# Kernel optimization log

Hardware: AMD Instinct MI355X
Metric: run time of the kernel (lower is better)

## Reference

```python
import jax, jax.numpy as jnp
import numpy as np

N_HEADS = 16
D_KV = 64
NUM_BUCKETS = 64      # bidirectional T5 buckets
MAX_DISTANCE = 50     # hist_step


def _rel_bucket(rel_pos):
    # T5 bidirectional relative-position bucketing.
    nb = NUM_BUCKETS // 2
    ret = (rel_pos > 0).astype(jnp.int32) * nb
    n = jnp.abs(rel_pos)
    max_exact = nb // 2
    is_small = n < max_exact
    large = max_exact + (
        jnp.log(jnp.maximum(n, 1).astype(jnp.float32) / max_exact)
        / np.log(MAX_DISTANCE / max_exact)
        * (nb - max_exact)
    ).astype(jnp.int32)
    large = jnp.minimum(large, nb - 1)
    return ret + jnp.where(is_small, n, large)


def _position_bias(rel_table, qlen, klen):
    ctx = jnp.arange(qlen)[:, None]
    mem = jnp.arange(klen)[None, :]
    bucket = _rel_bucket(mem - ctx)            # (q, k)
    vals = rel_table[bucket]                   # (q, k, h)
    return jnp.transpose(vals, (2, 0, 1))[None]  # (1, h, q, k)


def setup_inputs() -> dict:
    key = jax.random.key(0)
    ks = jax.random.split(key, 11)
    bs, qlen, d_model = 2, 2048, 1024
    inner = N_HEADS * D_KV
    s = 0.02
    return {
        "x": jax.random.normal(ks[0], (bs, qlen, d_model), jnp.float32),
        "Wq": jax.random.normal(ks[1], (d_model, inner), jnp.float32) * s,
        "bq": jnp.zeros((inner,), jnp.float32),
        "Wk": jax.random.normal(ks[2], (d_model, inner), jnp.float32) * s,
        "bk": jnp.zeros((inner,), jnp.float32),
        "Wv": jax.random.normal(ks[3], (d_model, inner), jnp.float32) * s,
        "bv": jnp.zeros((inner,), jnp.float32),
        "Wo": jax.random.normal(ks[4], (inner, d_model), jnp.float32) * s,
        "bo": jnp.zeros((d_model,), jnp.float32),
        "rel_table": jax.random.normal(ks[5], (NUM_BUCKETS, N_HEADS), jnp.float32) * s,
        "mask": jax.random.randint(ks[6], (bs, qlen), 0, 2) > 0,
    }


def reference(x, Wq, bq, Wk, bk, Wv, bv, Wo, bo, rel_table, mask):
    bs, qlen, d_model = x.shape

    def shape(h):  # (b, s, inner) -> (b, n, s, d)
        return h.reshape(bs, qlen, N_HEADS, D_KV).transpose(0, 2, 1, 3)

    q = shape(x @ Wq + bq)
    k = shape(x @ Wk + bk)
    v = shape(x @ Wv + bv)

    # No 1/sqrt(d) scaling in T5.
    scores = jnp.einsum('bnqd,bnkd->bnqk', q, k)

    mask_f = jnp.where(mask, -jnp.inf, 0.0).astype(scores.dtype)[:, None, None, :]  # (b,1,1,k)
    pos_bias = _position_bias(rel_table, qlen, qlen)  # (1,h,q,k)
    add = pos_bias + mask_f                           # bias + mask, broadcast over q

    weights = jax.nn.softmax(scores + add, axis=-1)   # dropout p=0 -> identity
    context = jnp.einsum('bnqk,bnkd->bnqd', weights, v)
    context = context.transpose(0, 2, 1, 3).reshape(bs, qlen, N_HEADS * D_KV)
    out = context @ Wo + bo
    return out, weights, pos_bias
```

## Files before the change

kernel.cpp:

```cpp
#include <hip/hip_runtime.h>
#include <math.h>

typedef _Float16 f16;
typedef f16 f16x8 __attribute__((ext_vector_type(8)));
typedef f16 f16x4 __attribute__((ext_vector_type(4)));
typedef float f32x4 __attribute__((ext_vector_type(4)));

#define W_OFF   (2*2048*1024)
#define PB_OFF  (W_OFF + 2LL*16*2048*2048)

#define NEG_BIG (-1.0e30f)

__device__ __forceinline__ int rel_bucket(int rel) {
    int ret = rel > 0 ? 32 : 0;
    int n = rel < 0 ? -rel : rel;
    if (n < 16) return ret + n;
    float fn = (float)n;
    float t = logf(fn * (1.0f / 16.0f));
    t = t / 1.1394343f;
    int large = 16 + (int)(t * 16.0f);
    if (large > 31) large = 31;
    return ret + large;
}


__global__ __launch_bounds__(256)
void conv_f16_kernel(const float* __restrict__ in, f16* __restrict__ out) {
    size_t i = ((size_t)blockIdx.x * 256 + threadIdx.x) * 4;
    float4 v = *(const float4*)&in[i];
    f16x4 h = { (f16)v.x, (f16)v.y, (f16)v.z, (f16)v.w };
    *(f16x4*)&out[i] = h;
}

__global__ __launch_bounds__(256)
void transpose_w_kernel(const float* __restrict__ W, f16* __restrict__ Wt) {
    __shared__ float tile[64 * 68];
    const int tid = threadIdx.x;
    const int bi = blockIdx.x, bj = blockIdx.y;
    #pragma unroll
    for (int it = 0; it < 4; ++it) {
        int slot = tid + it * 256;
        int row = slot >> 4, col4 = (slot & 15) * 4;
        float4 v = *(const float4*)&W[(size_t)(bi * 64 + row) * 1024 + bj * 64 + col4];
        *(float4*)&tile[row * 68 + col4] = v;
    }
    __syncthreads();
    #pragma unroll
    for (int it = 0; it < 4; ++it) {
        int slot = tid + it * 256;
        int nrow = slot >> 4, kcol4 = (slot & 15) * 4;
        f16x4 h;
        #pragma unroll
        for (int j = 0; j < 4; ++j)
            h[j] = (f16)tile[(kcol4 + j) * 68 + nrow];
        *(f16x4*)&Wt[(size_t)(bj * 64 + nrow) * 1024 + bi * 64 + kcol4] = h;
    }
}

__global__ __launch_bounds__(256)
void bias_tbl_kernel(const float* __restrict__ rel_table, float* __restrict__ tbl) {
    int idx = blockIdx.x * 256 + threadIdx.x;
    int h = idx >> 12, dd = idx & 4095;
    tbl[idx] = rel_table[rel_bucket(dd - 2047) * 16 + h];
}

__global__ __launch_bounds__(256)
void transpose_v_kernel(const f16* __restrict__ vh, f16* __restrict__ vt) {
    __shared__ f16 tile[64 * 72];
    const int tid = threadIdx.x;
    const int st = blockIdx.x, bh = blockIdx.y;
    #pragma unroll
    for (int it = 0; it < 2; ++it) {
        int slot = tid + it * 256;
        int row = slot >> 3, col8 = (slot & 7) * 8;
        f16x8 v = *(const f16x8*)&vh[((size_t)bh * 2048 + st * 64 + row) * 64 + col8];
        *(f16x8*)&tile[row * 72 + col8] = v;
    }
    __syncthreads();
    #pragma unroll
    for (int it = 0; it < 2; ++it) {
        int slot = tid + it * 256;
        int drow = slot >> 3, scol8 = (slot & 7) * 8;
        f16x8 r;
        #pragma unroll
        for (int j = 0; j < 8; ++j)
            r[j] = tile[(scol8 + j) * 72 + drow];
        *(f16x8*)&vt[((size_t)bh * 64 + drow) * 2048 + st * 64 + scol8] = r;
    }
}

__global__ __launch_bounds__(256)
void gemm_f16(const f16* __restrict__ A, const f16* __restrict__ Bt,
              const float* __restrict__ bias, void* __restrict__ Cout, int mode)
{
    __shared__ f16 aLDS[128 * 32];
    __shared__ f16 bLDS[128 * 32];
    const int tid = threadIdx.x;
    const int lane = tid & 63, wv = tid >> 6;
    const int quad = lane >> 4, l15 = lane & 15;
    const int wm = (wv & 1) * 64, wn = (wv >> 1) * 64;
    const int bm = blockIdx.y * 128, bn = blockIdx.x * 128;

    f32x4 acc[4][4];
    #pragma unroll
    for (int i = 0; i < 4; ++i)
        #pragma unroll
        for (int j = 0; j < 4; ++j)
            acc[i][j] = (f32x4){0.f, 0.f, 0.f, 0.f};

    for (int k0 = 0; k0 < 1024; k0 += 32) {
        __syncthreads();
        #pragma unroll
        for (int s = 0; s < 2; ++s) {
            int slot = tid + s * 256;
            int mt = slot >> 6, ln = slot & 63;
            int row = mt * 16 + (ln & 15), kk = (ln >> 4) * 8;
            float4 va = *(const float4*)&A[(size_t)(bm + row) * 1024 + k0 + kk];
            *(float4*)&aLDS[slot * 8] = va;
            float4 vb = *(const float4*)&Bt[(size_t)(bn + row) * 1024 + k0 + kk];
            *(float4*)&bLDS[slot * 8] = vb;
        }
        __syncthreads();
        f16x8 af[4], bf[4];
        #pragma unroll
        for (int i = 0; i < 4; ++i) {
            af[i] = *(const f16x8*)&aLDS[(((wm >> 4) + i) * 64 + lane) * 8];
            bf[i] = *(const f16x8*)&bLDS[(((wn >> 4) + i) * 64 + lane) * 8];
        }
        #pragma unroll
        for (int i = 0; i < 4; ++i)
            #pragma unroll
            for (int j = 0; j < 4; ++j)
                acc[i][j] = __builtin_amdgcn_mfma_f32_16x16x32_f16(af[i], bf[j], acc[i][j], 0, 0, 0);
    }

    #pragma unroll
    for (int j = 0; j < 4; ++j) {
        int n = bn + wn + j * 16 + l15;
        float bz = bias[n];
        #pragma unroll
        for (int i = 0; i < 4; ++i) {
            #pragma unroll
            for (int r = 0; r < 4; ++r) {
                int m = bm + wm + i * 16 + quad * 4 + r;
                float val = acc[i][j][r] + bz;
                if (mode == 0) {
                    ((float*)Cout)[(size_t)m * 1024 + n] = val;
                } else {
                    int b = m >> 11, srow = m & 2047, h = n >> 6, d = n & 63;
                    ((f16*)Cout)[(((size_t)(b * 16 + h) * 2048 + srow) << 6) + d] = (f16)val;
                }
            }
        }
    }
}

__global__ __launch_bounds__(256)
void attn_f16(const f16* __restrict__ qh, const f16* __restrict__ kh,
              const f16* __restrict__ vth, const float* __restrict__ tbl,
              const int* __restrict__ mask, float* __restrict__ wout,
              f16* __restrict__ ctxh)
{
    __shared__ float biasL[4096];
    __shared__ float maskL[2048];
    __shared__ f16 kL[8 * 64 * 8];
    __shared__ f16 vL[8 * 64 * 8];
    __shared__ f16 wnat[4 * 16 * 88];

    const int tid = threadIdx.x, lane = tid & 63, wv = tid >> 6;
    const int quad = lane >> 4, l15 = lane & 15;
    const int bh = blockIdx.y, b = bh >> 4, h = bh & 15;
    const int qt0 = blockIdx.x * 64;

    for (int i = tid; i < 1024; i += 256)
        *(float4*)&biasL[i * 4] = *(const float4*)&tbl[h * 4096 + i * 4];
    for (int i = tid; i < 512; i += 256) {
        int4 mv = *(const int4*)&mask[b * 2048 + i * 4];
        float4 f;
        f.x = mv.x ? NEG_BIG : 0.f;  f.y = mv.y ? NEG_BIG : 0.f;
        f.z = mv.z ? NEG_BIG : 0.f;  f.w = mv.w ? NEG_BIG : 0.f;
        *(float4*)&maskL[i * 4] = f;
    }

    const int q0 = qt0 + wv * 16;
    f16x8 aq[2];
    #pragma unroll
    for (int ds = 0; ds < 2; ++ds)
        aq[ds] = *(const f16x8*)&qh[((size_t)bh * 2048 + q0 + l15) * 64 + ds * 32 + quad * 8];
    __syncthreads();

    const int qrow_base = q0 + quad * 4;
    float lI[4] = {0.f, 0.f, 0.f, 0.f};

    for (int c = 0; c < 32; ++c) {
        __syncthreads();
        #pragma unroll
        for (int s = 0; s < 2; ++s) {
            int slot = tid + s * 256;
            int f = slot >> 6, ln = slot & 63;
            int dstep = f >> 2, nt = f & 3;
            int key = nt * 16 + (ln & 15);
            float4 v = *(const float4*)&kh[((size_t)bh * 2048 + c * 64 + key) * 64 + dstep * 32 + (ln >> 4) * 8];
            *(float4*)&kL[slot * 8] = v;
        }
        __syncthreads();
        #pragma unroll
        for (int nt = 0; nt < 4; ++nt) {
            f32x4 s4 = (f32x4){0.f, 0.f, 0.f, 0.f};
            #pragma unroll
            for (int ds = 0; ds < 2; ++ds) {
                f16x8 bf = *(const f16x8*)&kL[((ds * 4 + nt) * 64 + lane) * 8];
                s4 = __builtin_amdgcn_mfma_f32_16x16x32_f16(aq[ds], bf, s4, 0, 0, 0);
            }
            int k = c * 64 + nt * 16 + l15;
            float mk = maskL[k];
            #pragma unroll
            for (int r = 0; r < 4; ++r) {
                int q = qrow_base + r;
                float sc = s4[r] + biasL[k - q + 2047] + mk;
                lI[r] += __expf(sc - 20.f);
            }
        }
    }
    #pragma unroll
    for (int r = 0; r < 4; ++r) {
        float l = lI[r];
        l += __shfl_xor(l, 1, 64);
        l += __shfl_xor(l, 2, 64);
        l += __shfl_xor(l, 4, 64);
        l += __shfl_xor(l, 8, 64);
        lI[r] = 1.0f / l;
    }

    float* wbase = wout + (size_t)bh * 2048 * 2048;
    f32x4 oacc[4];
    #pragma unroll
    for (int nt = 0; nt < 4; ++nt) oacc[nt] = (f32x4){0.f, 0.f, 0.f, 0.f};

    for (int c = 0; c < 32; ++c) {
        __syncthreads();
        #pragma unroll
        for (int s = 0; s < 2; ++s) {
            int slot = tid + s * 256;
            int f = slot >> 6, ln = slot & 63;
            {
                int dstep = f >> 2, nt = f & 3;
                int key = nt * 16 + (ln & 15);
                float4 v = *(const float4*)&kh[((size_t)bh * 2048 + c * 64 + key) * 64 + dstep * 32 + (ln >> 4) * 8];
                *(float4*)&kL[slot * 8] = v;
            }
            {
                int ks = f >> 2, nt = f & 3;
                int d = nt * 16 + (ln & 15);
                float4 v = *(const float4*)&vth[((size_t)bh * 64 + d) * 2048 + c * 64 + ks * 32 + (ln >> 4) * 8];
                *(float4*)&vL[slot * 8] = v;
            }
        }
        __syncthreads();

        #pragma unroll
        for (int nt = 0; nt < 4; ++nt) {
            f32x4 s4 = (f32x4){0.f, 0.f, 0.f, 0.f};
            #pragma unroll
            for (int ds = 0; ds < 2; ++ds) {
                f16x8 bf = *(const f16x8*)&kL[((ds * 4 + nt) * 64 + lane) * 8];
                s4 = __builtin_amdgcn_mfma_f32_16x16x32_f16(aq[ds], bf, s4, 0, 0, 0);
            }
            int k = c * 64 + nt * 16 + l15;
            float mk = maskL[k];
            int key64 = nt * 16 + l15;
            #pragma unroll
            for (int r = 0; r < 4; ++r) {
                int q = qrow_base + r;
                float sc = s4[r] + biasL[k - q + 2047] + mk;
                float w = __expf(sc - 20.f) * lI[r];
                wbase[(size_t)q * 2048 + k] = w;
                wnat[wv * 1408 + (quad * 4 + r) * 88 + key64] = (f16)w;
            }
        }
        #pragma unroll
        for (int ks = 0; ks < 2; ++ks) {
            f16x8 wf = *(const f16x8*)&wnat[wv * 1408 + l15 * 88 + ks * 32 + quad * 8];
            #pragma unroll
            for (int nt = 0; nt < 4; ++nt) {
                f16x8 vf = *(const f16x8*)&vL[((ks * 4 + nt) * 64 + lane) * 8];
                oacc[nt] = __builtin_amdgcn_mfma_f32_16x16x32_f16(wf, vf, oacc[nt], 0, 0, 0);
            }
        }
    }

    #pragma unroll
    for (int nt = 0; nt < 4; ++nt) {
        int d = nt * 16 + l15;
        #pragma unroll
        for (int r = 0; r < 4; ++r) {
            int q = qrow_base + r;
            ctxh[((size_t)(b * 2048) + q) * 1024 + h * 64 + d] = (f16)oacc[nt][r];
        }
    }
}

__global__ __launch_bounds__(256)
void posbias_kernel(const float* __restrict__ rel_table, float* __restrict__ pb)
{
    size_t g = ((size_t)blockIdx.x * 256 + threadIdx.x) * 4;
    int k = (int)(g & 2047);
    int q = (int)((g >> 11) & 2047);
    int h = (int)(g >> 22);
    float4 r;
    float* rp = (float*)&r;
    #pragma unroll
    for (int j = 0; j < 4; ++j)
        rp[j] = rel_table[rel_bucket(k + j - q) * 16 + h];
    *(float4*)&pb[g] = r;
}

extern "C" void kernel_launch(void* const* d_in, const int* in_sizes, int n_in,
                              void* d_out, int out_size, void* d_ws, size_t ws_size,
                              hipStream_t stream) {
    const float* x    = (const float*)d_in[0];
    const float* Wq   = (const float*)d_in[1];
    const float* bq   = (const float*)d_in[2];
    const float* Wk   = (const float*)d_in[3];
    const float* bk   = (const float*)d_in[4];
    const float* Wv   = (const float*)d_in[5];
    const float* bv   = (const float*)d_in[6];
    const float* Wo   = (const float*)d_in[7];
    const float* bo   = (const float*)d_in[8];
    const float* rt   = (const float*)d_in[9];
    const int*   mask = (const int*)d_in[10];

    float* out = (float*)d_out;
    float* wts = out + W_OFF;
    float* pb  = out + PB_OFF;

    float* tbl  = pb;
    f16*   xh   = (f16*)(pb + 65536);
    f16*   wqt  = (f16*)(pb + 2162688);
    f16*   wkt  = (f16*)(pb + 2686976);
    f16*   wvt  = (f16*)(pb + 3211264);
    f16*   wot  = (f16*)(pb + 3735552);
    f16*   qh   = (f16*)(pb + 4259840);
    f16*   kh   = (f16*)(pb + 6356992);
    f16*   vh   = (f16*)(pb + 8454144);
    f16*   vth  = (f16*)(pb + 10551296);
    f16*   ctxh = (f16*)(pb + 12648448);

    dim3 blk(256);
    conv_f16_kernel<<<dim3(4096), blk, 0, stream>>>(x, xh);
    transpose_w_kernel<<<dim3(16, 16), blk, 0, stream>>>(Wq, wqt);
    transpose_w_kernel<<<dim3(16, 16), blk, 0, stream>>>(Wk, wkt);
    transpose_w_kernel<<<dim3(16, 16), blk, 0, stream>>>(Wv, wvt);
    transpose_w_kernel<<<dim3(16, 16), blk, 0, stream>>>(Wo, wot);
    bias_tbl_kernel<<<dim3(256), blk, 0, stream>>>(rt, tbl);

    gemm_f16<<<dim3(8, 32), blk, 0, stream>>>(xh, wqt, bq, qh, 1);
    gemm_f16<<<dim3(8, 32), blk, 0, stream>>>(xh, wkt, bk, kh, 1);
    gemm_f16<<<dim3(8, 32), blk, 0, stream>>>(xh, wvt, bv, vh, 1);
    transpose_v_kernel<<<dim3(32, 32), blk, 0, stream>>>(vh, vth);

    attn_f16<<<dim3(32, 32), blk, 0, stream>>>(qh, kh, vth, tbl, mask, wts, ctxh);

    gemm_f16<<<dim3(8, 32), blk, 0, stream>>>(ctxh, wot, bo, out, 0);
    posbias_kernel<<<dim3(65536), blk, 0, stream>>>(rt, pb);
}
```

Measured before the change: 1.153 ms.

## Fuse QKV GEMMs, use direct-to-LDS loads, drop attention LDS staging, remap blocks

The three Q/K/V projection GEMMs become one launch with a concatenated bias; this relies on wqt/wkt/wvt sitting contiguously in memory and on the output buffer offsets. The GEMM tile loads now use global_load_lds to write straight into LDS without going through registers. The attention kernel drops shared-memory K/V staging and its barriers, loading MFMA fragments directly from global memory into registers. It also swizzles the block index so that blocks sharing a head run together for L2 reuse, and folds the -20 shift into the mask constant. Risks are uncoalesced direct global fragment loads, with every wave re-reading K/V, and higher register pressure.

```diff
diff --git a/kernel.cpp b/kernel.cpp
--- a/kernel.cpp
+++ b/kernel.cpp
@@ -10,6 +10,13 @@
 #define PB_OFF  (W_OFF + 2LL*16*2048*2048)
 
 #define NEG_BIG (-1.0e30f)
+
+__device__ __forceinline__ void gload_lds16(const f16* g, f16* l) {
+    __builtin_amdgcn_global_load_lds(
+        (const __attribute__((address_space(1))) void*)g,
+        (__attribute__((address_space(3))) void*)l,
+        16, 0, 0);
+}
 
 __device__ __forceinline__ int rel_bucket(int rel) {
     int ret = rel > 0 ? 32 : 0;
@@ -65,6 +72,14 @@
 }
 
 __global__ __launch_bounds__(256)
+void concat_bias_kernel(const float* __restrict__ bq, const float* __restrict__ bk,
+                        const float* __restrict__ bv, float* __restrict__ o) {
+    int i = blockIdx.x * 256 + threadIdx.x;
+    float v = i < 1024 ? bq[i] : (i < 2048 ? bk[i - 1024] : bv[i - 2048]);
+    o[i] = v;
+}
+
+__global__ __launch_bounds__(256)
 void transpose_v_kernel(const f16* __restrict__ vh, f16* __restrict__ vt) {
     __shared__ f16 tile[64 * 72];
     const int tid = threadIdx.x;
@@ -112,13 +127,11 @@
         __syncthreads();
         #pragma unroll
         for (int s = 0; s < 2; ++s) {
-            int slot = tid + s * 256;
-            int mt = slot >> 6, ln = slot & 63;
-            int row = mt * 16 + (ln & 15), kk = (ln >> 4) * 8;
-            float4 va = *(const float4*)&A[(size_t)(bm + row) * 1024 + k0 + kk];
-            *(float4*)&aLDS[slot * 8] = va;
-            float4 vb = *(const float4*)&Bt[(size_t)(bn + row) * 1024 + k0 + kk];
-            *(float4*)&bLDS[slot * 8] = vb;
+            int row = (wv + s * 4) * 16 + l15;
+            gload_lds16(&A [(size_t)(bm + row) * 1024 + k0 + quad * 8],
+                        &aLDS[(size_t)(s * 256 + wv * 64) * 8]);
+            gload_lds16(&Bt[(size_t)(bn + row) * 1024 + k0 + quad * 8],
+                        &bLDS[(size_t)(s * 256 + wv * 64) * 8]);
         }
         __syncthreads();
         f16x8 af[4], bf[4];
@@ -147,8 +160,10 @@
                 if (mode == 0) {
                     ((float*)Cout)[(size_t)m * 1024 + n] = val;
                 } else {
-                    int b = m >> 11, srow = m & 2047, h = n >> 6, d = n & 63;
-                    ((f16*)Cout)[(((size_t)(b * 16 + h) * 2048 + srow) << 6) + d] = (f16)val;
+                    int b = m >> 11, srow = m & 2047;
+                    int buf = n >> 10, h = (n >> 6) & 15, d = n & 63;
+                    ((f16*)Cout)[(size_t)buf * 4194304 +
+                                 (((size_t)(b * 16 + h) * 2048 + srow) << 6) + d] = (f16)val;
                 }
             }
         }
@@ -163,22 +178,23 @@
 {
     __shared__ float biasL[4096];
     __shared__ float maskL[2048];
-    __shared__ f16 kL[8 * 64 * 8];
-    __shared__ f16 vL[8 * 64 * 8];
     __shared__ f16 wnat[4 * 16 * 88];
 
     const int tid = threadIdx.x, lane = tid & 63, wv = tid >> 6;
     const int quad = lane >> 4, l15 = lane & 15;
-    const int bh = blockIdx.y, b = bh >> 4, h = bh & 15;
-    const int qt0 = blockIdx.x * 64;
+
+    const int lin = blockIdx.y * 32 + blockIdx.x;
+    const int nl = (lin & 7) * 128 + (lin >> 3);
+    const int bh = nl >> 5, b = bh >> 4, h = bh & 15;
+    const int qt0 = (nl & 31) * 64;
 
     for (int i = tid; i < 1024; i += 256)
         *(float4*)&biasL[i * 4] = *(const float4*)&tbl[h * 4096 + i * 4];
     for (int i = tid; i < 512; i += 256) {
         int4 mv = *(const int4*)&mask[b * 2048 + i * 4];
         float4 f;
-        f.x = mv.x ? NEG_BIG : 0.f;  f.y = mv.y ? NEG_BIG : 0.f;
-        f.z = mv.z ? NEG_BIG : 0.f;  f.w = mv.w ? NEG_BIG : 0.f;
+        f.x = mv.x ? NEG_BIG : -20.f;  f.y = mv.y ? NEG_BIG : -20.f;
+        f.z = mv.z ? NEG_BIG : -20.f;  f.w = mv.w ? NEG_BIG : -20.f;
         *(float4*)&maskL[i * 4] = f;
     }
 
@@ -190,36 +206,30 @@
     __syncthreads();
 
     const int qrow_base = q0 + quad * 4;
+    const f16* kB = kh  + (size_t)bh * 2048 * 64 + quad * 8;
+    const f16* vB = vth + (size_t)bh * 64 * 2048 + quad * 8;
+
     float lI[4] = {0.f, 0.f, 0.f, 0.f};
 
     for (int c = 0; c < 32; ++c) {
-        __syncthreads();
-        #pragma unroll
-        for (int s = 0; s < 2; ++s) {
-            int slot = tid + s * 256;
-            int f = slot >> 6, ln = slot & 63;
-            int dstep = f >> 2, nt = f & 3;
-            int key = nt * 16 + (ln & 15);
-            float4 v = *(const float4*)&kh[((size_t)bh * 2048 + c * 64 + key) * 64 + dstep * 32 + (ln >> 4) * 8];
-            *(float4*)&kL[slot * 8] = v;
-        }
-        __syncthreads();
+        f16x8 bf[2][4];
+        #pragma unroll
+        for (int nt = 0; nt < 4; ++nt) {
+            const f16* kp = kB + (size_t)(c * 64 + nt * 16 + l15) * 64;
+            bf[0][nt] = *(const f16x8*)&kp[0];
+            bf[1][nt] = *(const f16x8*)&kp[32];
+        }
         #pragma unroll
         for (int nt = 0; nt < 4; ++nt) {
             f32x4 s4 = (f32x4){0.f, 0.f, 0.f, 0.f};
-            #pragma unroll
-            for (int ds = 0; ds < 2; ++ds) {
-                f16x8 bf = *(const f16x8*)&kL[((ds * 4 + nt) * 64 + lane) * 8];
-                s4 = __builtin_amdgcn_mfma_f32_16x16x32_f16(aq[ds], bf, s4, 0, 0, 0);
-            }
+            s4 = __builtin_amdgcn_mfma_f32_16x16x32_f16(aq[0], bf[0][nt], s4, 0, 0, 0);
+            s4 = __builtin_amdgcn_mfma_f32_16x16x32_f16(aq[1], bf[1][nt], s4, 0, 0, 0);
             int k = c * 64 + nt * 16 + l15;
             float mk = maskL[k];
-            #pragma unroll
-            for (int r = 0; r < 4; ++r) {
-                int q = qrow_base + r;
-                float sc = s4[r] + biasL[k - q + 2047] + mk;
-                lI[r] += __expf(sc - 20.f);
-            }
+            int bi = k - qrow_base + 2047;
+            #pragma unroll
+            for (int r = 0; r < 4; ++r)
+                lI[r] += __expf(s4[r] + biasL[bi - r] + mk);
         }
     }
     #pragma unroll
@@ -238,54 +248,43 @@
     for (int nt = 0; nt < 4; ++nt) oacc[nt] = (f32x4){0.f, 0.f, 0.f, 0.f};
 
     for (int c = 0; c < 32; ++c) {
-        __syncthreads();
-        #pragma unroll
-        for (int s = 0; s < 2; ++s) {
-            int slot = tid + s * 256;
-            int f = slot >> 6, ln = slot & 63;
-            {
-                int dstep = f >> 2, nt = f & 3;
-                int key = nt * 16 + (ln & 15);
-                float4 v = *(const float4*)&kh[((size_t)bh * 2048 + c * 64 + key) * 64 + dstep * 32 + (ln >> 4) * 8];
-                *(float4*)&kL[slot * 8] = v;
-            }
-            {
-                int ks = f >> 2, nt = f & 3;
-                int d = nt * 16 + (ln & 15);
-                float4 v = *(const float4*)&vth[((size_t)bh * 64 + d) * 2048 + c * 64 + ks * 32 + (ln >> 4) * 8];
-                *(float4*)&vL[slot * 8] = v;
-            }
-        }
-        __syncthreads();
+        f16x8 bf[2][4];
+        #pragma unroll
+        for (int nt = 0; nt < 4; ++nt) {
+            const f16* kp = kB + (size_t)(c * 64 + nt * 16 + l15) * 64;
+            bf[0][nt] = *(const f16x8*)&kp[0];
+            bf[1][nt] = *(const f16x8*)&kp[32];
+        }
+        f16x8 vf[2][4];
+        #pragma unroll
+        for (int nt = 0; nt < 4; ++nt) {
+            const f16* vp = vB + (size_t)(nt * 16 + l15) * 2048 + c * 64;
+            vf[0][nt] = *(const f16x8*)&vp[0];
+            vf[1][nt] = *(const f16x8*)&vp[32];
+        }
 
         #pragma unroll
         for (int nt = 0; nt < 4; ++nt) {
             f32x4 s4 = (f32x4){0.f, 0.f, 0.f, 0.f};
-            #pragma unroll
-            for (int ds = 0; ds < 2; ++ds) {
-                f16x8 bf = *(const f16x8*)&kL[((ds * 4 + nt) * 64 + lane) * 8];
-                s4 = __builtin_amdgcn_mfma_f32_16x16x32_f16(aq[ds], bf, s4, 0, 0, 0);
-            }
+            s4 = __builtin_amdgcn_mfma_f32_16x16x32_f16(aq[0], bf[0][nt], s4, 0, 0, 0);
+            s4 = __builtin_amdgcn_mfma_f32_16x16x32_f16(aq[1], bf[1][nt], s4, 0, 0, 0);
             int k = c * 64 + nt * 16 + l15;
             float mk = maskL[k];
-            int key64 = nt * 16 + l15;
+            int bi = k - qrow_base + 2047;
+            float* wp = wbase + (size_t)qrow_base * 2048 + k;
             #pragma unroll
             for (int r = 0; r < 4; ++r) {
-                int q = qrow_base + r;
-                float sc = s4[r] + biasL[k - q + 2047] + mk;
-                float w = __expf(sc - 20.f) * lI[r];
-                wbase[(size_t)q * 2048 + k] = w;
-                wnat[wv * 1408 + (quad * 4 + r) * 88 + key64] = (f16)w;
+                float w = __expf(s4[r] + biasL[bi - r] + mk) * lI[r];
+                wp[(size_t)r * 2048] = w;
+                wnat[wv * 1408 + (quad * 4 + r) * 88 + nt * 16 + l15] = (f16)w;
             }
         }
         #pragma unroll
         for (int ks = 0; ks < 2; ++ks) {
             f16x8 wf = *(const f16x8*)&wnat[wv * 1408 + l15 * 88 + ks * 32 + quad * 8];
             #pragma unroll
-            for (int nt = 0; nt < 4; ++nt) {
-                f16x8 vf = *(const f16x8*)&vL[((ks * 4 + nt) * 64 + lane) * 8];
-                oacc[nt] = __builtin_amdgcn_mfma_f32_16x16x32_f16(wf, vf, oacc[nt], 0, 0, 0);
-            }
+            for (int nt = 0; nt < 4; ++nt)
+                oacc[nt] = __builtin_amdgcn_mfma_f32_16x16x32_f16(wf, vf[ks][nt], oacc[nt], 0, 0, 0);
         }
     }
 
@@ -345,6 +344,7 @@
     f16*   vh   = (f16*)(pb + 8454144);
     f16*   vth  = (f16*)(pb + 10551296);
     f16*   ctxh = (f16*)(pb + 12648448);
+    float* bqkv = pb + 14745600;
 
     dim3 blk(256);
     conv_f16_kernel<<<dim3(4096), blk, 0, stream>>>(x, xh);
@@ -353,10 +353,9 @@
     transpose_w_kernel<<<dim3(16, 16), blk, 0, stream>>>(Wv, wvt);
     transpose_w_kernel<<<dim3(16, 16), blk, 0, stream>>>(Wo, wot);
     bias_tbl_kernel<<<dim3(256), blk, 0, stream>>>(rt, tbl);
-
-    gemm_f16<<<dim3(8, 32), blk, 0, stream>>>(xh, wqt, bq, qh, 1);
-    gemm_f16<<<dim3(8, 32), blk, 0, stream>>>(xh, wkt, bk, kh, 1);
-    gemm_f16<<<dim3(8, 32), blk, 0, stream>>>(xh, wvt, bv, vh, 1);
+    concat_bias_kernel<<<dim3(12), blk, 0, stream>>>(bq, bk, bv, bqkv);
+
+    gemm_f16<<<dim3(24, 32), blk, 0, stream>>>(xh, wqt, bqkv, qh, 1);
     transpose_v_kernel<<<dim3(32, 32), blk, 0, stream>>>(vh, vth);
 
     attn_f16<<<dim3(32, 32), blk, 0, stream>>>(qh, kh, vth, tbl, mask, wts, ctxh);
```

After: 1.259 ms. 1.09x slower.
